# Kernel optimization log

Hardware: AMD Instinct MI355X
Metric: run time of the kernel (lower is better)

The kernel has to match this reference:

```python
import jax, jax.numpy as jnp
import numpy as np

N = 50000
E = 800000
D = 512
H = 256
K = 16
COLLAPSE_REG = 1.0


def setup_inputs() -> dict:
    key = jax.random.key(0)
    ks = jax.random.split(key, 8)
    embeddings = jax.random.normal(ks[0], (N, D), dtype=jnp.float32)
    edge_src = jax.random.randint(ks[1], (E,), 0, N, dtype=jnp.int32)
    edge_dst = jax.random.randint(ks[2], (E,), 0, N, dtype=jnp.int32)
    # GCNConv params (glorot-ish scaling)
    W1 = jax.random.normal(ks[3], (D, H), dtype=jnp.float32) / np.sqrt(D)
    b1 = jnp.zeros((H,), dtype=jnp.float32)
    W2 = jax.random.normal(ks[4], (H, H), dtype=jnp.float32) / np.sqrt(H)
    b2 = jnp.zeros((H,), dtype=jnp.float32)
    Wa = jax.random.normal(ks[5], (H, K), dtype=jnp.float32) / np.sqrt(H)
    ba = jnp.zeros((K,), dtype=jnp.float32)
    return {"embeddings": embeddings, "edge_src": edge_src, "edge_dst": edge_dst,
            "W1": W1, "b1": b1, "W2": W2, "b2": b2, "Wa": Wa, "ba": ba}


def _gcn_conv(x, W, b, src, dst, dis):
    # PyG GCNConv: transform then D^{-1/2}(A+I)D^{-1/2} aggregation + bias.
    x = x @ W                                   # [N, out]
    norm = dis[src] * dis[dst]                  # [E]
    agg = jax.ops.segment_sum(x[src] * norm[:, None], dst, num_segments=N)
    agg = agg + (dis * dis)[:, None] * x        # self-loop term
    return agg + b


def reference(embeddings, edge_src, edge_dst, W1, b1, W2, b2, Wa, ba):
    # symmetric-norm degrees with self-loops (edge weight 1)
    deg = 1.0 + jax.ops.segment_sum(jnp.ones((E,), jnp.float32), edge_dst, num_segments=N)
    dis = jax.lax.rsqrt(deg)                    # deg > 0 always (self-loop)

    x = jax.nn.selu(_gcn_conv(embeddings, W1, b1, edge_src, edge_dst, dis))
    x_skip = x  # dropout is identity in eval
    x = jax.nn.selu(_gcn_conv(x, W2, b2, edge_src, edge_dst, dis))
    x = x + x_skip
    assignments = jax.nn.softmax(x @ Wa + ba, axis=1)   # [N, K]

    # ---- DMoN losses (faithful to original, incl. scalar normalizer) ----
    degrees = jax.ops.segment_sum(jnp.ones((E,), jnp.float32), edge_src, num_segments=N)  # row sums of A
    m = degrees.sum() / 2.0
    AS = jax.ops.segment_sum(assignments[edge_dst], edge_src, num_segments=N)  # A @ S, [N, K]
    trace_pooled = jnp.sum(assignments * AS)    # trace(S^T A S)
    dS = degrees @ assignments                  # [K]
    normalizer = jnp.dot(dS, dS) / (2.0 * m)    # scalar (as in original code)
    spectral_loss = -(trace_pooled - K * normalizer) / (2.0 * m)

    cluster_sizes = assignments.sum(axis=0)     # [K]
    collapse_loss = jnp.linalg.norm(cluster_sizes) / N * jnp.sqrt(jnp.float32(K)) - 1.0
    entropy = -jnp.sum(assignments * jnp.log(assignments + 1e-8)) / N
    entropy_loss = -0.1 * entropy
    total_loss = spectral_loss + COLLAPSE_REG * collapse_loss + entropy_loss

    pooled = (assignments / (cluster_sizes + 1e-8)).T @ embeddings  # [K, D]
    return (assignments, pooled, spectral_loss, COLLAPSE_REG * collapse_loss, total_loss, entropy_loss)
```

## Files before the change

kernel.cpp:

```cpp
#include <hip/hip_runtime.h>
#include <hip/hip_fp16.h>
#include <math.h>

#define NN 50000
#define EE 800000
#define DD 512
#define HH 256
#define KK 16
#define NB_SCAN 196

typedef _Float16 half8_t __attribute__((ext_vector_type(8)));
typedef float f32x4 __attribute__((ext_vector_type(4)));

__global__ void zero_kernel(int* __restrict__ p, int n) {
    int i = blockIdx.x * blockDim.x + threadIdx.x;
    if (i < n) p[i] = 0;
}

__global__ void count_kernel(const int4* __restrict__ src4, const int4* __restrict__ dst4,
                             int* __restrict__ indeg, int* __restrict__ outdeg) {
    int e = blockIdx.x * blockDim.x + threadIdx.x;
    if (e < EE / 4) {
        int4 s = src4[e], d = dst4[e];
        atomicAdd(&outdeg[s.x], 1); atomicAdd(&outdeg[s.y], 1);
        atomicAdd(&outdeg[s.z], 1); atomicAdd(&outdeg[s.w], 1);
        atomicAdd(&indeg[d.x], 1);  atomicAdd(&indeg[d.y], 1);
        atomicAdd(&indeg[d.z], 1);  atomicAdd(&indeg[d.w], 1);
    }
}

__global__ void scan_p1(const int* __restrict__ in, int* __restrict__ part, int n,
                        const int* __restrict__ outdeg, float* __restrict__ dis,
                        float* __restrict__ degf) {
    __shared__ int tile[256];
    int t = threadIdx.x;
    int i = blockIdx.x * 256 + t;
    int v = (i < n) ? in[i] : 0;
    tile[t] = v;
    if (i < n) {
        dis[i]  = 1.0f / sqrtf(1.0f + (float)v);
        degf[i] = (float)outdeg[i];
    }
    __syncthreads();
    for (int o = 128; o > 0; o >>= 1) {
        if (t < o) tile[t] += tile[t + o];
        __syncthreads();
    }
    if (t == 0) part[blockIdx.x] = tile[0];
}

__global__ void scan_p2(int* __restrict__ part, int nb, int* __restrict__ off_end) {
    __shared__ int tile[256];
    int t = threadIdx.x;
    int v = (t < nb) ? part[t] : 0;
    tile[t] = v;
    __syncthreads();
    for (int o = 1; o < 256; o <<= 1) {
        int x = (t >= o) ? tile[t - o] : 0;
        __syncthreads();
        tile[t] += x;
        __syncthreads();
    }
    if (t < nb) part[t] = tile[t] - v;
    if (t == 255) *off_end = tile[255];
}

__global__ void scan_p3(const int* __restrict__ in, const int* __restrict__ part,
                        int* __restrict__ out, int n) {
    __shared__ int tile[256];
    int t = threadIdx.x;
    int i = blockIdx.x * 256 + t;
    int v = (i < n) ? in[i] : 0;
    tile[t] = v;
    __syncthreads();
    for (int o = 1; o < 256; o <<= 1) {
        int x = (t >= o) ? tile[t - o] : 0;
        __syncthreads();
        tile[t] += x;
        __syncthreads();
    }
    if (i < n) out[i] = part[blockIdx.x] + tile[t] - v;
}

__global__ void scatter_kernel(const int4* __restrict__ src4, const int4* __restrict__ dst4,
                               const int* __restrict__ off, int* __restrict__ cur,
                               const float* __restrict__ dis,
                               int* __restrict__ nbr, __half* __restrict__ wgt) {
    int e = blockIdx.x * blockDim.x + threadIdx.x;
    if (e < EE / 4) {
        int4 s = src4[e], d = dst4[e];
        int p, q;
        p = atomicAdd(&cur[d.x], 1); q = off[d.x] + p;
        nbr[q] = s.x; wgt[q] = __float2half(dis[s.x] * dis[d.x]);
        p = atomicAdd(&cur[d.y], 1); q = off[d.y] + p;
        nbr[q] = s.y; wgt[q] = __float2half(dis[s.y] * dis[d.y]);
        p = atomicAdd(&cur[d.z], 1); q = off[d.z] + p;
        nbr[q] = s.z; wgt[q] = __float2half(dis[s.z] * dis[d.z]);
        p = atomicAdd(&cur[d.w], 1); q = off[d.w] + p;
        nbr[q] = s.w; wgt[q] = __float2half(dis[s.w] * dis[d.w]);
    }
}

__global__ void transpose_w(const float* __restrict__ W1, __half* __restrict__ Wt1,
                            const float* __restrict__ W2, __half* __restrict__ Wt2,
                            const float* __restrict__ Wa, __half* __restrict__ WaT) {
    int i = blockIdx.x * 256 + threadIdx.x;
    if (i < DD * HH) {
        int k = i / HH, n = i % HH;
        Wt1[(size_t)n * DD + k] = __float2half(W1[i]);
    } else if (i < DD * HH + HH * HH) {
        int j = i - DD * HH;
        int k = j / HH, n = j % HH;
        Wt2[(size_t)n * HH + k] = __float2half(W2[j]);
    } else if (i < DD * HH + HH * HH + HH * KK) {
        int j = i - DD * HH - HH * HH;
        int k = j / KK, n = j % KK;
        WaT[n * HH + k] = __float2half(Wa[j]);
    }
}

__device__ inline half8_t loadfrag(const float* p) {
    float4 x0 = *(const float4*)p;
    float4 x1 = *(const float4*)(p + 4);
    half8_t h;
    h[0] = (_Float16)x0.x; h[1] = (_Float16)x0.y;
    h[2] = (_Float16)x0.z; h[3] = (_Float16)x0.w;
    h[4] = (_Float16)x1.x; h[5] = (_Float16)x1.y;
    h[6] = (_Float16)x1.z; h[7] = (_Float16)x1.w;
    return h;
}
__device__ inline half8_t loadfrag(const __half* p) { return *(const half8_t*)p; }

template <typename TA, int KDIM>
__global__ __launch_bounds__(256) void mfma_gemm(const TA* __restrict__ A,
                                                 const __half* __restrict__ Bt,
                                                 __half* __restrict__ C, int M) {
    constexpr int KI = KDIM / 32;
    int t = threadIdx.x;
    int wave = t >> 6, lane = t & 63, quad = lane >> 4, l16 = lane & 15;
    int row0 = blockIdx.x * 128, col0 = blockIdx.y * 128;
    int wm = (wave & 1) * 64, wn = (wave >> 1) * 64;

    const TA* ap[4];
    const __half* bp[4];
#pragma unroll
    for (int mi = 0; mi < 4; mi++) {
        int r = row0 + wm + mi * 16 + l16;
        if (r >= M) r = M - 1;
        ap[mi] = A + (size_t)r * KDIM + quad * 8;
    }
#pragma unroll
    for (int ni = 0; ni < 4; ni++)
        bp[ni] = Bt + (size_t)(col0 + wn + ni * 16 + l16) * KDIM + quad * 8;

    f32x4 acc[4][4] = {};
    half8_t af[4], bf[4], afn[4], bfn[4];
#pragma unroll
    for (int mi = 0; mi < 4; mi++) af[mi] = loadfrag(ap[mi]);
#pragma unroll
    for (int ni = 0; ni < 4; ni++) bf[ni] = loadfrag(bp[ni]);

#pragma unroll
    for (int i = 0; i < KI; i++) {
        if (i + 1 < KI) {
#pragma unroll
            for (int mi = 0; mi < 4; mi++) afn[mi] = loadfrag(ap[mi] + (i + 1) * 32);
#pragma unroll
            for (int ni = 0; ni < 4; ni++) bfn[ni] = loadfrag(bp[ni] + (i + 1) * 32);
        }
#pragma unroll
        for (int mi = 0; mi < 4; mi++)
#pragma unroll
            for (int ni = 0; ni < 4; ni++)
                acc[mi][ni] = __builtin_amdgcn_mfma_f32_16x16x32_f16(
                    af[mi], bf[ni], acc[mi][ni], 0, 0, 0);
        if (i + 1 < KI) {
#pragma unroll
            for (int mi = 0; mi < 4; mi++) af[mi] = afn[mi];
#pragma unroll
            for (int ni = 0; ni < 4; ni++) bf[ni] = bfn[ni];
        }
    }

#pragma unroll
    for (int mi = 0; mi < 4; mi++) {
#pragma unroll
        for (int r = 0; r < 4; r++) {
            int rr = row0 + wm + mi * 16 + quad * 4 + r;
            if (rr < M) {
#pragma unroll
                for (int ni = 0; ni < 4; ni++) {
                    C[(size_t)rr * HH + col0 + wn + ni * 16 + l16] =
                        __float2half(acc[mi][ni][r]);
                }
            }
        }
    }
}

__device__ inline void fma8(float* acc, uint4 raw, float w) {
    const __half2* h = (const __half2*)&raw;
#pragma unroll
    for (int i = 0; i < 4; i++) {
        float2 f = __half22float2(h[i]);
        acc[2 * i]     += w * f.x;
        acc[2 * i + 1] += w * f.y;
    }
}

__global__ __launch_bounds__(256) void agg_selu(const __half* __restrict__ T,
                                                const float* __restrict__ dis,
                                                const int* __restrict__ off,
                                                const int* __restrict__ nbr,
                                                const __half* __restrict__ wgt,
                                                const float* __restrict__ bias,
                                                const __half* skip, __half* out) {
    int t = threadIdx.x;
    int l32 = t & 31;
    int n = blockIdx.x * 8 + (t >> 5);
    int c = l32 * 8;
    float dn = dis[n];

    float acc[8];
#pragma unroll
    for (int i = 0; i < 8; i++) acc[i] = 0.f;
    fma8(acc, *(const uint4*)(T + (size_t)n * HH + c), dn * dn);

    int s0 = off[n], s1 = off[n + 1];
    for (int base = s0; base < s1; base += 32) {
        int cnt = min(32, s1 - base);
        int sidv = 0; float wv = 0.f;
        if (l32 < cnt) {
            sidv = nbr[base + l32];
            wv = __half2float(wgt[base + l32]);
        }
        int j = 0;
        for (; j + 8 <= cnt; j += 8) {
            int a0 = __shfl(sidv, j, 32),     a1 = __shfl(sidv, j + 1, 32);
            int a2 = __shfl(sidv, j + 2, 32), a3 = __shfl(sidv, j + 3, 32);
            int a4 = __shfl(sidv, j + 4, 32), a5 = __shfl(sidv, j + 5, 32);
            int a6 = __shfl(sidv, j + 6, 32), a7 = __shfl(sidv, j + 7, 32);
            float w0 = __shfl(wv, j, 32),     w1 = __shfl(wv, j + 1, 32);
            float w2 = __shfl(wv, j + 2, 32), w3 = __shfl(wv, j + 3, 32);
            float w4 = __shfl(wv, j + 4, 32), w5 = __shfl(wv, j + 5, 32);
            float w6 = __shfl(wv, j + 6, 32), w7 = __shfl(wv, j + 7, 32);
            uint4 r0 = *(const uint4*)(T + (size_t)a0 * HH + c);
            uint4 r1 = *(const uint4*)(T + (size_t)a1 * HH + c);
            uint4 r2 = *(const uint4*)(T + (size_t)a2 * HH + c);
            uint4 r3 = *(const uint4*)(T + (size_t)a3 * HH + c);
            uint4 r4 = *(const uint4*)(T + (size_t)a4 * HH + c);
            uint4 r5 = *(const uint4*)(T + (size_t)a5 * HH + c);
            uint4 r6 = *(const uint4*)(T + (size_t)a6 * HH + c);
            uint4 r7 = *(const uint4*)(T + (size_t)a7 * HH + c);
            fma8(acc, r0, w0); fma8(acc, r1, w1);
            fma8(acc, r2, w2); fma8(acc, r3, w3);
            fma8(acc, r4, w4); fma8(acc, r5, w5);
            fma8(acc, r6, w6); fma8(acc, r7, w7);
        }
        for (; j < cnt; j++) {
            int s = __shfl(sidv, j, 32);
            float w = __shfl(wv, j, 32);
            fma8(acc, *(const uint4*)(T + (size_t)s * HH + c), w);
        }
    }

    const float scale = 1.0507009873554805f;
    const float alpha = 1.6732632423543772f;
    float4 b0 = *(const float4*)(bias + c);
    float4 b1 = *(const float4*)(bias + c + 4);
    float bb[8] = {b0.x, b0.y, b0.z, b0.w, b1.x, b1.y, b1.z, b1.w};
    float sk8[8];
#pragma unroll
    for (int i = 0; i < 8; i++) sk8[i] = 0.f;
    if (skip) {
        uint4 raw = *(const uint4*)(skip + (size_t)n * HH + c);
        const __half2* h = (const __half2*)&raw;
#pragma unroll
        for (int i = 0; i < 4; i++) {
            float2 f = __half22float2(h[i]);
            sk8[2 * i] = f.x; sk8[2 * i + 1] = f.y;
        }
    }
    _Float16 res[8];
#pragma unroll
    for (int i = 0; i < 8; i++) {
        float v = acc[i] + bb[i];
        float r = v > 0.f ? scale * v : scale * alpha * expm1f(v);
        res[i] = (_Float16)(r + sk8[i]);
    }
    *(uint4*)(out + (size_t)n * HH + c) = *(uint4*)res;
}

__global__ __launch_bounds__(256) void assign_mfma(const __half* __restrict__ Hb,
                                                   const __half* __restrict__ WaT,
                                                   const float* __restrict__ ba,
                                                   const float* __restrict__ degf,
                                                   float* __restrict__ out_assign,
                                                   __half* __restrict__ out_f16,
                                                   float* __restrict__ scal) {
    int t = threadIdx.x;
    int wave = t >> 6, lane = t & 63, quad = lane >> 4, l16 = lane & 15;
    int nb = blockIdx.x * 256 + wave * 64;

    f32x4 acc[4] = {};
    const __half* bp = WaT + l16 * HH + quad * 8;
    const __half* ap[4];
#pragma unroll
    for (int mi = 0; mi < 4; mi++) {
        int r = nb + mi * 16 + l16;
        if (r >= NN) r = NN - 1;
        ap[mi] = Hb + (size_t)r * HH + quad * 8;
    }
#pragma unroll
    for (int s = 0; s < 8; s++) {
        half8_t bf = *(const half8_t*)(bp + s * 32);
#pragma unroll
        for (int mi = 0; mi < 4; mi++) {
            half8_t af = *(const half8_t*)(ap[mi] + s * 32);
            acc[mi] = __builtin_amdgcn_mfma_f32_16x16x32_f16(af, bf, acc[mi], 0, 0, 0);
        }
    }

    float myb = ba[l16];
    float lcs = 0.f, ldS = 0.f, lent = 0.f;
#pragma unroll
    for (int mi = 0; mi < 4; mi++) {
#pragma unroll
        for (int r = 0; r < 4; r++) {
            int node = nb + mi * 16 + quad * 4 + r;
            bool ok = node < NN;
            float logit = acc[mi][r] + myb;
            float mx = logit;
            for (int o = 1; o < 16; o <<= 1) mx = fmaxf(mx, __shfl_xor(mx, o, 16));
            float e = expf(logit - mx);
            float sum = e;
            for (int o = 1; o < 16; o <<= 1) sum += __shfl_xor(sum, o, 16);
            float a = e / sum;
            if (ok) {
                out_assign[(size_t)node * KK + l16] = a;
                out_f16[(size_t)node * KK + l16] = __float2half(a);
                lcs += a;
                ldS += degf[node] * a;
                lent += a * logf(a + 1e-8f);
            }
        }
    }
    lcs += __shfl_xor(lcs, 16); lcs += __shfl_xor(lcs, 32);
    ldS += __shfl_xor(ldS, 16); ldS += __shfl_xor(ldS, 32);
    for (int o = 32; o >= 1; o >>= 1) lent += __shfl_xor(lent, o);
    if (quad == 0) {
        atomicAdd(&scal[l16], lcs);
        atomicAdd(&scal[16 + l16], ldS);
    }
    if (lane == 0) atomicAdd(&scal[33], lent);
}

__device__ inline float dot16h(const __half* a, const __half* b) {
    uint4 a0 = *(const uint4*)a, a1 = *(const uint4*)(a + 8);
    uint4 b0 = *(const uint4*)b, b1 = *(const uint4*)(b + 8);
    float p = 0.f;
    const __half2* xa = (const __half2*)&a0;
    const __half2* xb = (const __half2*)&b0;
#pragma unroll
    for (int i = 0; i < 4; i++) {
        float2 u = __half22float2(xa[i]), v = __half22float2(xb[i]);
        p += u.x * v.x + u.y * v.y;
    }
    xa = (const __half2*)&a1; xb = (const __half2*)&b1;
#pragma unroll
    for (int i = 0; i < 4; i++) {
        float2 u = __half22float2(xa[i]), v = __half22float2(xb[i]);
        p += u.x * v.x + u.y * v.y;
    }
    return p;
}

__global__ __launch_bounds__(256) void edge_trace(const int4* __restrict__ src4,
                                                  const int4* __restrict__ dst4,
                                                  const __half* __restrict__ Ah,
                                                  float* __restrict__ scal) {
    int e = blockIdx.x * blockDim.x + threadIdx.x;
    float p = 0.f;
    if (e < EE / 4) {
        int4 s = src4[e], d = dst4[e];
        p += dot16h(Ah + (size_t)s.x * KK, Ah + (size_t)d.x * KK);
        p += dot16h(Ah + (size_t)s.y * KK, Ah + (size_t)d.y * KK);
        p += dot16h(Ah + (size_t)s.z * KK, Ah + (size_t)d.z * KK);
        p += dot16h(Ah + (size_t)s.w * KK, Ah + (size_t)d.w * KK);
    }
    for (int o = 32; o >= 1; o >>= 1) p += __shfl_xor(p, o);
    __shared__ float sp;
    if (threadIdx.x == 0) sp = 0.f;
    __syncthreads();
    if ((threadIdx.x & 63) == 0) atomicAdd(&sp, p);
    __syncthreads();
    if (threadIdx.x == 0) atomicAdd(&scal[32], sp);
}

#define PCH 125
__global__ __launch_bounds__(256) void pooled_partial(const float* __restrict__ emb,
                                                      const float* __restrict__ assign,
                                                      float* __restrict__ pool_acc) {
    int d = blockIdx.x * 256 + threadIdx.x;
    int c0 = blockIdx.y * PCH;
    float acc[KK];
#pragma unroll
    for (int k = 0; k < KK; k++) acc[k] = 0.f;
    __shared__ float sa[PCH * KK];
    {
        const float4* srcv = (const float4*)(assign + (size_t)c0 * KK);
        float4* dstv = (float4*)sa;
        for (int i = threadIdx.x; i < PCH * KK / 4; i += 256) dstv[i] = srcv[i];
    }
    __syncthreads();
    for (int j = 0; j < PCH; j++) {
        float ev = emb[(size_t)(c0 + j) * DD + d];
#pragma unroll
        for (int k4 = 0; k4 < 4; k4++) {
            float4 s4 = *(const float4*)&sa[j * KK + k4 * 4];
            acc[k4 * 4 + 0] += s4.x * ev;
            acc[k4 * 4 + 1] += s4.y * ev;
            acc[k4 * 4 + 2] += s4.z * ev;
            acc[k4 * 4 + 3] += s4.w * ev;
        }
    }
#pragma unroll
    for (int k = 0; k < KK; k++) atomicAdd(&pool_acc[k * DD + d], acc[k]);
}

__global__ void finalize(const float* __restrict__ pool_acc, const float* __restrict__ scal,
                         float* __restrict__ out) {
    int bx = blockIdx.x, t = threadIdx.x;
    if (bx < 32) {
        int i = bx * 256 + t;
        int k = i / DD;
        out[800000 + i] = pool_acc[i] / (scal[k] + 1e-8f);
    } else if (t == 0) {
        float cs2 = 0.f, ds2 = 0.f;
        for (int k = 0; k < KK; k++) {
            cs2 += scal[k] * scal[k];
            ds2 += scal[16 + k] * scal[16 + k];
        }
        float two_m = (float)EE;
        float normalizer = ds2 / two_m;
        float trace = scal[32];
        float spectral = -(trace - (float)KK * normalizer) / two_m;
        float collapse = sqrtf(cs2) / (float)NN * 4.0f - 1.0f;
        float entl = 0.1f * scal[33] / (float)NN;
        out[808192] = spectral;
        out[808193] = collapse;
        out[808194] = spectral + collapse + entl;
        out[808195] = entl;
    }
}

extern "C" void kernel_launch(void* const* d_in, const int* in_sizes, int n_in,
                              void* d_out, int out_size, void* d_ws, size_t ws_size,
                              hipStream_t stream) {
    const float* emb = (const float*)d_in[0];
    const int* esrc  = (const int*)d_in[1];
    const int* edst  = (const int*)d_in[2];
    const float* W1  = (const float*)d_in[3];
    const float* b1  = (const float*)d_in[4];
    const float* W2  = (const float*)d_in[5];
    const float* b2  = (const float*)d_in[6];
    const float* Wa  = (const float*)d_in[7];
    const float* ba  = (const float*)d_in[8];
    float* out = (float*)d_out;

    int* indeg      = (int*)d_ws;
    int* outdeg     = indeg + 50000;
    int* cur        = outdeg + 50000;
    float* pool_acc = (float*)(cur + 50000);
    float* scal     = pool_acc + 8192;
    int* part       = (int*)(scal + 64);
    int* off        = part + 256;
    int* nbr        = off + 50004;
    float* dis      = (float*)(nbr + 800000);
    float* degf     = dis + 50000;
    __half* wgt     = (__half*)(degf + 50000);
    __half* Wt1     = wgt + 800000;
    __half* Wt2     = Wt1 + 256 * 512;
    __half* WaT     = Wt2 + 256 * 256;
    __half* T       = WaT + 16 * 256;
    __half* Hb      = T + (size_t)NN * HH;
    __half* Ah      = T;

    zero_kernel<<<dim3(619), 256, 0, stream>>>((int*)d_ws, 158256);
    count_kernel<<<dim3(782), 256, 0, stream>>>((const int4*)esrc, (const int4*)edst,
                                                indeg, outdeg);

    scan_p1<<<dim3(NB_SCAN), 256, 0, stream>>>(indeg, part, NN, outdeg, dis, degf);
    scan_p2<<<dim3(1), 256, 0, stream>>>(part, NB_SCAN, off + NN);
    scan_p3<<<dim3(NB_SCAN), 256, 0, stream>>>(indeg, part, off, NN);
    scatter_kernel<<<dim3(782), 256, 0, stream>>>((const int4*)esrc, (const int4*)edst,
                                                  off, cur, dis, nbr, wgt);

    transpose_w<<<dim3(784), 256, 0, stream>>>(W1, Wt1, W2, Wt2, Wa, WaT);

    mfma_gemm<float, DD><<<dim3(392, 2), 256, 0, stream>>>(emb, Wt1, T, NN);
    agg_selu<<<dim3(6250), 256, 0, stream>>>(T, dis, off, nbr, wgt, b1, nullptr, Hb);

    mfma_gemm<__half, HH><<<dim3(392, 2), 256, 0, stream>>>(Hb, Wt2, T, NN);
    agg_selu<<<dim3(6250), 256, 0, stream>>>(T, dis, off, nbr, wgt, b2, Hb, Hb);

    assign_mfma<<<dim3(196), 256, 0, stream>>>(Hb, WaT, ba, degf, out, Ah, scal);
    edge_trace<<<dim3(782), 256, 0, stream>>>((const int4*)esrc, (const int4*)edst, Ah, scal);
    pooled_partial<<<dim3(2, 400), 256, 0, stream>>>(emb, out, pool_acc);
    finalize<<<dim3(33), 256, 0, stream>>>(pool_acc, scal, out);
}
```

Measured before the change: 618.1 us.

## Stage A tile through double-buffered LDS in MFMA GEMM

The A operand is now loaded cooperatively into a double-buffered shared-memory tile, with each thread converting 16 elements to fp16 once, so waves stop reading and converting their own A fragments from global memory. Before, each wave read its A rows directly, so the two waves sharing rows duplicated both the loads and the fp32-to-fp16 conversions. The change adds LDS traffic and a block barrier on every k-step. The B operand is still read per-wave straight from global memory.

```diff
diff --git a/kernel.cpp b/kernel.cpp
--- a/kernel.cpp
+++ b/kernel.cpp
@@ -119,67 +119,93 @@
     }
 }
 
-__device__ inline half8_t loadfrag(const float* p) {
-    float4 x0 = *(const float4*)p;
-    float4 x1 = *(const float4*)(p + 4);
-    half8_t h;
-    h[0] = (_Float16)x0.x; h[1] = (_Float16)x0.y;
-    h[2] = (_Float16)x0.z; h[3] = (_Float16)x0.w;
-    h[4] = (_Float16)x1.x; h[5] = (_Float16)x1.y;
-    h[6] = (_Float16)x1.z; h[7] = (_Float16)x1.w;
-    return h;
-}
-__device__ inline half8_t loadfrag(const __half* p) { return *(const half8_t*)p; }
-
 template <typename TA, int KDIM>
 __global__ __launch_bounds__(256) void mfma_gemm(const TA* __restrict__ A,
                                                  const __half* __restrict__ Bt,
                                                  __half* __restrict__ C, int M) {
+    constexpr bool F32 = sizeof(TA) == 4;
     constexpr int KI = KDIM / 32;
+    __shared__ _Float16 As[2][128 * 40];
+
     int t = threadIdx.x;
     int wave = t >> 6, lane = t & 63, quad = lane >> 4, l16 = lane & 15;
     int row0 = blockIdx.x * 128, col0 = blockIdx.y * 128;
     int wm = (wave & 1) * 64, wn = (wave >> 1) * 64;
-
-    const TA* ap[4];
-    const __half* bp[4];
-#pragma unroll
-    for (int mi = 0; mi < 4; mi++) {
-        int r = row0 + wm + mi * 16 + l16;
-        if (r >= M) r = M - 1;
-        ap[mi] = A + (size_t)r * KDIM + quad * 8;
-    }
+    int sr = t >> 1, sk = (t & 1) * 16;
+
+    int gr = row0 + sr;
+    if (gr >= M) gr = M - 1;
+    const TA* aptr = A + (size_t)gr * KDIM + sk;
+
+    const __half* brow[4];
 #pragma unroll
     for (int ni = 0; ni < 4; ni++)
-        bp[ni] = Bt + (size_t)(col0 + wn + ni * 16 + l16) * KDIM + quad * 8;
+        brow[ni] = Bt + (size_t)(col0 + wn + ni * 16 + l16) * KDIM + quad * 8;
 
     f32x4 acc[4][4] = {};
-    half8_t af[4], bf[4], afn[4], bfn[4];
-#pragma unroll
-    for (int mi = 0; mi < 4; mi++) af[mi] = loadfrag(ap[mi]);
-#pragma unroll
-    for (int ni = 0; ni < 4; ni++) bf[ni] = loadfrag(bp[ni]);
+    uint4 areg[2], bcur[4];
+
+    auto gloadA = [&](int k0, uint4* o) {
+        if constexpr (F32) {
+            float4 x0 = *(const float4*)(aptr + k0);
+            float4 x1 = *(const float4*)(aptr + k0 + 4);
+            float4 x2 = *(const float4*)(aptr + k0 + 8);
+            float4 x3 = *(const float4*)(aptr + k0 + 12);
+            _Float16 h[16];
+            h[0] = (_Float16)x0.x;  h[1] = (_Float16)x0.y;
+            h[2] = (_Float16)x0.z;  h[3] = (_Float16)x0.w;
+            h[4] = (_Float16)x1.x;  h[5] = (_Float16)x1.y;
+            h[6] = (_Float16)x1.z;  h[7] = (_Float16)x1.w;
+            h[8] = (_Float16)x2.x;  h[9] = (_Float16)x2.y;
+            h[10] = (_Float16)x2.z; h[11] = (_Float16)x2.w;
+            h[12] = (_Float16)x3.x; h[13] = (_Float16)x3.y;
+            h[14] = (_Float16)x3.z; h[15] = (_Float16)x3.w;
+            o[0] = *(uint4*)h;
+            o[1] = *(uint4*)(h + 8);
+        } else {
+            o[0] = *(const uint4*)(aptr + k0);
+            o[1] = *(const uint4*)(aptr + k0 + 8);
+        }
+    };
+    auto sstore = [&](int buf, const uint4* v) {
+        *(uint4*)&As[buf][sr * 40 + sk] = v[0];
+        *(uint4*)&As[buf][sr * 40 + sk + 8] = v[1];
+    };
+
+    gloadA(0, areg);
+#pragma unroll
+    for (int ni = 0; ni < 4; ni++) bcur[ni] = *(const uint4*)(brow[ni]);
+    sstore(0, areg);
+    __syncthreads();
 
 #pragma unroll
     for (int i = 0; i < KI; i++) {
+        int cur = i & 1;
+        uint4 anext[2], bnext[4];
         if (i + 1 < KI) {
-#pragma unroll
-            for (int mi = 0; mi < 4; mi++) afn[mi] = loadfrag(ap[mi] + (i + 1) * 32);
-#pragma unroll
-            for (int ni = 0; ni < 4; ni++) bfn[ni] = loadfrag(bp[ni] + (i + 1) * 32);
-        }
+            gloadA((i + 1) * 32, anext);
+#pragma unroll
+            for (int ni = 0; ni < 4; ni++)
+                bnext[ni] = *(const uint4*)(brow[ni] + (i + 1) * 32);
+        }
+
+        half8_t af[4];
+#pragma unroll
+        for (int mi = 0; mi < 4; mi++)
+            af[mi] = *(const half8_t*)&As[cur][(wm + mi * 16 + l16) * 40 + quad * 8];
 #pragma unroll
         for (int mi = 0; mi < 4; mi++)
 #pragma unroll
             for (int ni = 0; ni < 4; ni++)
                 acc[mi][ni] = __builtin_amdgcn_mfma_f32_16x16x32_f16(
-                    af[mi], bf[ni], acc[mi][ni], 0, 0, 0);
+                    af[mi], *(half8_t*)&bcur[ni], acc[mi][ni], 0, 0, 0);
+
         if (i + 1 < KI) {
-#pragma unroll
-            for (int mi = 0; mi < 4; mi++) af[mi] = afn[mi];
-#pragma unroll
-            for (int ni = 0; ni < 4; ni++) bf[ni] = bfn[ni];
-        }
+            sstore(cur ^ 1, anext);
+#pragma unroll
+            for (int ni = 0; ni < 4; ni++) bcur[ni] = bnext[ni];
+        }
+        __syncthreads();
     }
 
 #pragma unroll
```

New measurement: 563.9 us. 1.1x faster.
